# Kernel tuning notes

Hardware: AMD Instinct MI355X
Metric: run time of the kernel (lower is better)

The kernel has to match this reference:

```python
import jax, jax.numpy as jnp
import numpy as np

EPS = 1e-5
K = 9
DILATION = 1

def bn(x, g, b, m, v):
    # x: (B,C,N,1), inference-mode BatchNorm2d with running stats
    sh = (1, -1, 1, 1)
    return (x - m.reshape(sh)) * (g.reshape(sh) / jnp.sqrt(v.reshape(sh) + EPS)) + b.reshape(sh)

def conv1x1(x, w, b):
    # w: (Cout, Cin), x: (B,Cin,N,1)
    return jnp.einsum('oc,bcnj->bonj', w, x) + b.reshape(1, -1, 1, 1)

def knn_idx(feat, k):
    # feat: (B,C,N) -> (B,N,k) indices of k nearest nodes (incl. self)
    xt = jnp.transpose(feat, (0, 2, 1))  # (B,N,C)
    x2 = jnp.sum(xt * xt, axis=-1)       # (B,N)
    dist = x2[:, :, None] - 2.0 * jnp.einsum('bnc,bmc->bnm', xt, xt) + x2[:, None, :]
    _, idx = jax.lax.top_k(-dist, k)
    return idx

def setup_inputs():
    key = jax.random.key(0)
    ks = jax.random.split(key, 24)
    B, C, H, W = 16, 256, 32, 32
    HID = 512
    def g(i, shape, s=1.0):
        return jax.random.normal(ks[i], shape, dtype=jnp.float32) * s
    def pos(i, shape):
        return jax.random.uniform(ks[i], shape, dtype=jnp.float32, minval=0.5, maxval=1.5)
    return {
        'x': g(0, (B, C, H, W)),
        'fc1_w': g(1, (C, C), 0.05), 'fc1_b': g(2, (C,), 0.05),
        'bn1_g': pos(3, (C,)), 'bn1_b': g(4, (C,), 0.1), 'bn1_m': g(5, (C,), 0.1), 'bn1_v': pos(6, (C,)),
        'gc_w': g(7, (HID, 2 * C), 0.05), 'gc_b': g(8, (HID,), 0.05),
        'gbn_g': pos(9, (HID,)), 'gbn_b': g(10, (HID,), 0.1), 'gbn_m': g(11, (HID,), 0.1), 'gbn_v': pos(12, (HID,)),
        'bn2_g': pos(13, (HID,)), 'bn2_b': g(14, (HID,), 0.1), 'bn2_m': g(15, (HID,), 0.1), 'bn2_v': pos(16, (HID,)),
        'fc2_w': g(17, (C, HID), 0.05), 'fc2_b': g(18, (C,), 0.05),
        'bn3_g': pos(19, (C,)), 'bn3_b': g(20, (C,), 0.1), 'bn3_m': g(21, (C,), 0.1), 'bn3_v': pos(22, (C,)),
    }

def reference(x, fc1_w, fc1_b, bn1_g, bn1_b, bn1_m, bn1_v,
              gc_w, gc_b, gbn_g, gbn_b, gbn_m, gbn_v,
              bn2_g, bn2_b, bn2_m, bn2_v,
              fc2_w, fc2_b, bn3_g, bn3_b, bn3_m, bn3_v):
    B, C, H, W = x.shape
    N = H * W
    x = x.reshape(B, C, N, 1)
    shortcut = x
    # fc1: 1x1 conv + BN
    h = bn(conv1x1(x, fc1_w, fc1_b), bn1_g, bn1_b, bn1_m, bn1_v)
    # DyGraphConv2d: dynamic dilated kNN graph over N nodes
    feat = h[..., 0]  # (B,C,N)
    idx = knn_idx(feat, K * DILATION)[:, :, ::DILATION]  # (B,N,K)
    # MRConv2d: max over neighbors of (x_j - x_i)
    x_j = jax.vmap(lambda f, i: f[:, i])(feat, idx)        # (B,C,N,K) gather
    diff_max = jnp.max(x_j - feat[:, :, :, None], axis=-1)  # (B,C,N)
    # interleave [x, max_diff] along channel dim -> (B, 2C, N, 1)
    m = jnp.stack([feat, diff_max], axis=2).reshape(B, 2 * C, N, 1)
    g = conv1x1(m, gc_w, gc_b)
    g = bn(g, gbn_g, gbn_b, gbn_m, gbn_v)  # BasicConv BN, act='None'
    # graph_conv Sequential: BN + GELU (erf, torch default)
    g = jax.nn.gelu(bn(g, bn2_g, bn2_b, bn2_m, bn2_v), approximate=False)
    # fc2 + residual (drop_path=0 -> identity)
    out = bn(conv1x1(g, fc2_w, fc2_b), bn3_g, bn3_b, bn3_m, bn3_v)
    return out + shortcut
```

## Files before the change

### kernel.cpp

```cpp
#include <hip/hip_runtime.h>
#include <hip/hip_bf16.h>
#include <stdint.h>

typedef unsigned long long u64;
typedef __hip_bfloat16 bf16;
typedef short s8v __attribute__((ext_vector_type(8)));
typedef short s4v __attribute__((ext_vector_type(4)));
typedef float f4v __attribute__((ext_vector_type(4)));

#define B_   16
#define C_   256
#define N_   1024
#define HID_ 512

__device__ __forceinline__ unsigned short f2b(float f) {
    unsigned u = __float_as_uint(f);
    unsigned r = (u + 0x7FFFu + ((u >> 16) & 1u)) >> 16;
    return (unsigned short)r;
}
__device__ __forceinline__ float b2f(unsigned short s) {
    return __uint_as_float(((unsigned)s) << 16);
}
__device__ __forceinline__ float ldIn(const void* p, long long i, int bf) {
    return bf ? b2f(((const unsigned short*)p)[i]) : ((const float*)p)[i];
}
__device__ __forceinline__ u64 shfl_xor_u64(u64 v, int m) {
    unsigned lo = (unsigned)v, hi = (unsigned)(v >> 32);
    lo = __shfl_xor(lo, m, 64);
    hi = __shfl_xor(hi, m, 64);
    return ((u64)hi << 32) | lo;
}

__global__ void prep_kernel(const void* xp,
    const void* fc1_b, const void* bn1_g, const void* bn1_b, const void* bn1_m, const void* bn1_v,
    const void* gc_b,  const void* gbn_g, const void* gbn_b, const void* gbn_m, const void* gbn_v,
    const void* bn2_g, const void* bn2_b, const void* bn2_m, const void* bn2_v,
    const void* fc2_b, const void* bn3_g, const void* bn3_b, const void* bn3_m, const void* bn3_v,
    int* flags, float* s1, float* t1, float* Sg, float* Tg, float* s3, float* t3,
    float* x2)
{
    __shared__ int sf;
    if (threadIdx.x == 0) {
        const unsigned short* u = (const unsigned short*)xp;
        int cnt = 0;
        for (int i = 0; i < 64; ++i) {
            int e = (u[2 * i] >> 7) & 0xFF;
            cnt += (e >= 87 && e <= 167);
        }
        int f = (cnt >= 48) ? 1 : 0;
        flags[0] = f;
        sf = f;
    }
    for (int i = threadIdx.x; i < B_ * N_; i += 512) x2[i] = 0.f;
    __syncthreads();
    int bf = sf;
    int i = threadIdx.x;
    if (i < 256) {
        float g = ldIn(bn1_g, i, bf), bb = ldIn(bn1_b, i, bf);
        float m = ldIn(bn1_m, i, bf), v  = ldIn(bn1_v, i, bf);
        float s = g / sqrtf(v + 1e-5f);
        s1[i] = s;
        t1[i] = (ldIn(fc1_b, i, bf) - m) * s + bb;

        float g3 = ldIn(bn3_g, i, bf), b3 = ldIn(bn3_b, i, bf);
        float m3 = ldIn(bn3_m, i, bf), v3 = ldIn(bn3_v, i, bf);
        float ss3 = g3 / sqrtf(v3 + 1e-5f);
        s3[i] = ss3;
        t3[i] = (ldIn(fc2_b, i, bf) - m3) * ss3 + b3;
    }
    if (i < 512) {
        float gg = ldIn(gbn_g, i, bf), gb = ldIn(gbn_b, i, bf);
        float gm = ldIn(gbn_m, i, bf), gv = ldIn(gbn_v, i, bf);
        float sg = gg / sqrtf(gv + 1e-5f);
        float g2 = ldIn(bn2_g, i, bf), b2 = ldIn(bn2_b, i, bf);
        float m2 = ldIn(bn2_m, i, bf), v2 = ldIn(bn2_v, i, bf);
        float s2 = g2 / sqrtf(v2 + 1e-5f);
        Sg[i] = sg * s2;
        Tg[i] = ((ldIn(gc_b, i, bf) - gm) * sg + gb - m2) * s2 + b2;
    }
}

__global__ __launch_bounds__(256)
void cast_weights(const void* w1, const void* wg, const void* w2,
                  short* W1b, short* Wgb, short* W2b, const int* flags)
{
    int inf = flags[0];
    int i = blockIdx.x * 256 + threadIdx.x;
    if (i < 65536) {
        W1b[i] = (short)f2b(ldIn(w1, i, inf));
    } else if (i < 65536 + 262144) {
        int j = i - 65536;
        Wgb[j] = (short)f2b(ldIn(wg, j, inf));
    } else {
        int j = i - 327680;
        W2b[j] = (short)f2b(ldIn(w2, j, inf));
    }
}

__global__ __launch_bounds__(256)
void fc1_valu(const void* __restrict__ Aw, const void* __restrict__ Bx,
              float* __restrict__ Ft, short* __restrict__ Fhi,
              short* __restrict__ Flo, float* __restrict__ x2,
              const float* __restrict__ s1, const float* __restrict__ t1,
              const int* __restrict__ flags)
{
    __shared__ float As[16][68];
    __shared__ float Bs[16][68];
    __shared__ float x2part[16][64];

    int inf = flags[0];
    int b  = blockIdx.z;
    int o0 = blockIdx.y * 64, n0 = blockIdx.x * 64;
    int t  = threadIdx.x;
    int tn = t & 15, to = t >> 4;
    long long bbase = (long long)b * C_ * N_;

    float acc[4][4] = {};

    for (int k0 = 0; k0 < C_; k0 += 16) {
        {
            int l = t * 4;
            int ao = l >> 4, ak = l & 15;
            long long ai = (long long)(o0 + ao) * C_ + k0 + ak;
            As[ak + 0][ao] = ldIn(Aw, ai + 0, inf);
            As[ak + 1][ao] = ldIn(Aw, ai + 1, inf);
            As[ak + 2][ao] = ldIn(Aw, ai + 2, inf);
            As[ak + 3][ao] = ldIn(Aw, ai + 3, inf);
        }
        {
            int l = t * 4;
            int bk = l >> 6, bn = l & 63;
            long long bi = bbase + (long long)(k0 + bk) * N_ + n0 + bn;
            Bs[bk][bn + 0] = ldIn(Bx, bi + 0, inf);
            Bs[bk][bn + 1] = ldIn(Bx, bi + 1, inf);
            Bs[bk][bn + 2] = ldIn(Bx, bi + 2, inf);
            Bs[bk][bn + 3] = ldIn(Bx, bi + 3, inf);
        }
        __syncthreads();
        #pragma unroll
        for (int k = 0; k < 16; ++k) {
            float av[4], bv[4];
            #pragma unroll
            for (int i = 0; i < 4; ++i) av[i] = As[k][to * 4 + i];
            #pragma unroll
            for (int j = 0; j < 4; ++j) bv[j] = Bs[k][tn * 4 + j];
            #pragma unroll
            for (int i = 0; i < 4; ++i)
                #pragma unroll
                for (int j = 0; j < 4; ++j) acc[i][j] += av[i] * bv[j];
        }
        __syncthreads();
    }

    float p2[4] = {};
    #pragma unroll
    for (int i = 0; i < 4; ++i) {
        int o = o0 + to * 4 + i;
        float s = s1[o], tt = t1[o];
        #pragma unroll
        for (int j = 0; j < 4; ++j) {
            int n = n0 + tn * 4 + j;
            float f = acc[i][j] * s + tt;
            long long oi = ((long long)(b << 10) + n) * C_ + o;
            Ft[oi] = f;
            unsigned short h = f2b(f);
            Fhi[oi] = (short)h;
            Flo[oi] = (short)f2b(f - b2f(h));
            p2[j] += f * f;
        }
    }
    #pragma unroll
    for (int j = 0; j < 4; ++j) x2part[to][tn * 4 + j] = p2[j];
    __syncthreads();
    if (t < 64) {
        float s = 0.f;
        #pragma unroll
        for (int r = 0; r < 16; ++r) s += x2part[r][t];
        atomicAdd(&x2[(b << 10) + n0 + t], s);
    }
}

__global__ __launch_bounds__(256)
void gram_topk(const short* __restrict__ Fhi, const short* __restrict__ Flo,
               const float* __restrict__ x2, u64* __restrict__ Part)
{
    __shared__ __align__(16) char ldsbuf[31232];
    short* Ah  = (short*)(ldsbuf);
    short* Al  = (short*)(ldsbuf + 10240);
    short* Bh  = (short*)(ldsbuf + 20480);
    short* Bl  = (short*)(ldsbuf + 25600);
    float* x2s = (float*)(ldsbuf + 30720);
    u64*   mrg  = (u64*)(ldsbuf);
    u64*   mrg2 = (u64*)(ldsbuf + 20480);

    int t = threadIdx.x;
    int q0 = blockIdx.x * 64, mq = blockIdx.y, b = blockIdx.z;
    int wv = t >> 6, ln15 = t & 15, quad = (t >> 4) & 3;

    if (t < 128) x2s[t] = x2[(b << 10) + mq * 128 + t];

    f4v acc[8];
    #pragma unroll
    for (int i = 0; i < 8; ++i) acc[i] = 0.f;

    for (int kc = 0; kc < 8; ++kc) {
        __syncthreads();
        #pragma unroll
        for (int s = 0; s < 6; ++s) {
            int sid = t + s * 256;
            int row = sid >> 2, seg = sid & 3;
            const short* src;
            short* dst;
            int grow;
            if (row < 128)      { dst = &Ah[row * 40 + seg * 8];         grow = mq * 128 + row;       src = Fhi; }
            else if (row < 256) { dst = &Al[(row - 128) * 40 + seg * 8]; grow = mq * 128 + row - 128; src = Flo; }
            else if (row < 320) { dst = &Bh[(row - 256) * 40 + seg * 8]; grow = q0 + row - 256;       src = Fhi; }
            else                { dst = &Bl[(row - 320) * 40 + seg * 8]; grow = q0 + row - 320;       src = Flo; }
            *(s8v*)dst = *(const s8v*)(src + ((long long)((b << 10) + grow)) * C_ + kc * 32 + seg * 8);
        }
        __syncthreads();
        s8v qh = *(s8v*)&Bh[(wv * 16 + ln15) * 40 + quad * 8];
        s8v ql = *(s8v*)&Bl[(wv * 16 + ln15) * 40 + quad * 8];
        #pragma unroll
        for (int i = 0; i < 8; ++i) {
            s8v mh = *(s8v*)&Ah[(i * 16 + ln15) * 40 + quad * 8];
            s8v ml = *(s8v*)&Al[(i * 16 + ln15) * 40 + quad * 8];
            acc[i] = __builtin_amdgcn_mfma_f32_16x16x32_bf16(mh, qh, acc[i], 0, 0, 0);
            acc[i] = __builtin_amdgcn_mfma_f32_16x16x32_bf16(mh, ql, acc[i], 0, 0, 0);
            acc[i] = __builtin_amdgcn_mfma_f32_16x16x32_bf16(ml, qh, acc[i], 0, 0, 0);
        }
    }

    u64 l[9];
    #pragma unroll
    for (int i = 0; i < 9; ++i) l[i] = ~0ULL;
    #pragma unroll
    for (int i = 0; i < 8; ++i) {
        #pragma unroll
        for (int r = 0; r < 4; ++r) {
            int mloc = i * 16 + quad * 4 + r;
            float d = x2s[mloc] - 2.f * acc[i][r];
            unsigned u = __float_as_uint(d);
            u = (u & 0x80000000u) ? ~u : (u | 0x80000000u);
            u64 key = ((u64)u << 32) | (unsigned)(mq * 128 + mloc);
            if (key < l[8]) {
                u64 x = key;
                #pragma unroll
                for (int jj = 0; jj < 9; ++jj) {
                    u64 lo2 = l[jj] < x ? l[jj] : x;
                    u64 hi2 = l[jj] < x ? x : l[jj];
                    l[jj] = lo2; x = hi2;
                }
            }
        }
    }

    __syncthreads();
    {
        int qloc = wv * 16 + ln15;
        #pragma unroll
        for (int k = 0; k < 9; ++k) mrg[(qloc * 4 + quad) * 9 + k] = l[k];
    }
    __syncthreads();
    if (t < 128) {
        int r = t >> 1, pr = t & 1;
        const u64* LA = &mrg[(r * 4 + pr * 2) * 9];
        const u64* LB = LA + 9;
        int ia = 0, ib = 0;
        u64* Po = &mrg2[(r * 2 + pr) * 9];
        #pragma unroll
        for (int k = 0; k < 9; ++k) {
            u64 va = LA[ia], vb = LB[ib];
            bool ta = va < vb;
            Po[k] = ta ? va : vb;
            ia += ta; ib += !ta;
        }
    }
    __syncthreads();
    if (t < 64) {
        const u64* LA = &mrg2[(t * 2) * 9];
        const u64* LB = LA + 9;
        int ia = 0, ib = 0;
        u64* P = Part + (((long long)((b << 10) + q0 + t)) * 8 + mq) * 9;
        #pragma unroll
        for (int k = 0; k < 9; ++k) {
            u64 va = LA[ia], vb = LB[ib];
            bool ta = va < vb;
            P[k] = ta ? va : vb;
            ia += ta; ib += !ta;
        }
    }
}

__global__ __launch_bounds__(256)
void build_Mt(const float* __restrict__ Ft, const u64* __restrict__ Part,
              short* __restrict__ Mt)
{
    int t = threadIdx.x;
    int wv = t >> 6, lane = t & 63;
    int n = blockIdx.x * 4 + wv;
    int b = blockIdx.y;
    long long nb = (long long)(b << 10) + n;

    const u64* L = Part + nb * 72 + (long long)(lane & 7) * 9;
    u64 l[9];
    #pragma unroll
    for (int k = 0; k < 9; ++k) l[k] = L[k];
    #pragma unroll
    for (int s = 1; s <= 4; s <<= 1) {
        u64 p[9];
        #pragma unroll
        for (int k = 0; k < 9; ++k) p[k] = shfl_xor_u64(l[k], s);
        #pragma unroll
        for (int k = 0; k < 9; ++k) {
            u64 x = p[k];
            if (x < l[8]) {
                #pragma unroll
                for (int jj = 0; jj < 9; ++jj) {
                    u64 lo2 = l[jj] < x ? l[jj] : x;
                    u64 hi2 = l[jj] < x ? x : l[jj];
                    l[jj] = lo2; x = hi2;
                }
            }
        }
    }

    int c0 = lane * 4;
    f4v f = *(const f4v*)(Ft + nb * C_ + c0);
    f4v mx = {-3.4e38f, -3.4e38f, -3.4e38f, -3.4e38f};
    #pragma unroll
    for (int k = 0; k < 9; ++k) {
        int id = (int)(l[k] & 0xFFFFFFFFu);
        f4v g = *(const f4v*)(Ft + ((long long)(b << 10) + id) * C_ + c0);
        mx[0] = fmaxf(mx[0], g[0]); mx[1] = fmaxf(mx[1], g[1]);
        mx[2] = fmaxf(mx[2], g[2]); mx[3] = fmaxf(mx[3], g[3]);
    }
    s8v m8;
    #pragma unroll
    for (int r = 0; r < 4; ++r) {
        m8[2 * r]     = (short)f2b(f[r]);
        m8[2 * r + 1] = (short)f2b(mx[r] - f[r]);
    }
    *(s8v*)(Mt + nb * (2 * C_) + 2 * c0) = m8;
}

template<int EPI>
__global__ __launch_bounds__(256)
void mfma_gemm(const short* __restrict__ A, const short* __restrict__ Bm,
               void* __restrict__ Out, const float* __restrict__ scale,
               const float* __restrict__ bias, const void* __restrict__ resid,
               const int* __restrict__ flags, int K, int Odim)
{
    __shared__ short As[128][40];
    __shared__ short Bs[128][40];

    int t = threadIdx.x, b = blockIdx.z;
    int n0 = blockIdx.x * 128, o0 = blockIdx.y * 128;
    int wv = t >> 6, ln = t & 15, quad = (t >> 4) & 3;
    int wo = (wv & 1) * 64, wn = (wv >> 1) * 64;

    f4v acc[4][4];
    #pragma unroll
    for (int i = 0; i < 4; ++i)
        #pragma unroll
        for (int j = 0; j < 4; ++j) acc[i][j] = 0.f;

    const short* Ab = A + (long long)o0 * K;
    const short* Bb = Bm + ((long long)(b << 10) + n0) * K;

    for (int k0 = 0; k0 < K; k0 += 32) {
        __syncthreads();
        #pragma unroll
        for (int s = 0; s < 2; ++s) {
            int sid = t + s * 256;
            int row = sid >> 2, seg = sid & 3;
            *(s8v*)&As[row][seg * 8] = *(const s8v*)(Ab + (long long)row * K + k0 + seg * 8);
            *(s8v*)&Bs[row][seg * 8] = *(const s8v*)(Bb + (long long)row * K + k0 + seg * 8);
        }
        __syncthreads();
        s8v a[4], bf[4];
        #pragma unroll
        for (int i = 0; i < 4; ++i) a[i]  = *(s8v*)&As[wo + i * 16 + ln][quad * 8];
        #pragma unroll
        for (int j = 0; j < 4; ++j) bf[j] = *(s8v*)&Bs[wn + j * 16 + ln][quad * 8];
        #pragma unroll
        for (int i = 0; i < 4; ++i)
            #pragma unroll
            for (int j = 0; j < 4; ++j)
                acc[i][j] = __builtin_amdgcn_mfma_f32_16x16x32_bf16(a[i], bf[j], acc[i][j], 0, 0, 0);
    }

    int inf = flags[0];
    #pragma unroll
    for (int i = 0; i < 4; ++i) {
        int ob = o0 + wo + i * 16 + quad * 4;
        #pragma unroll
        for (int j = 0; j < 4; ++j) {
            int n = n0 + wn + j * 16 + ln;
            f4v v = acc[i][j];
            if (EPI == 0) {
                s4v g;
                #pragma unroll
                for (int r = 0; r < 4; ++r) {
                    float val = v[r] * scale[ob + r] + bias[ob + r];
                    val = 0.5f * val * (1.0f + erff(val * 0.70710678118654752f));
                    g[r] = (short)f2b(val);
                }
                *(s4v*)((short*)Out + ((long long)(b << 10) + n) * Odim + ob) = g;
            } else {
                #pragma unroll
                for (int r = 0; r < 4; ++r) {
                    int o = ob + r;
                    long long oi = ((long long)b * Odim + o) * N_ + n;
                    ((float*)Out)[oi] = v[r] * scale[o] + bias[o] + ldIn(resid, oi, inf);
                }
            }
        }
    }
}

extern "C" void kernel_launch(void* const* d_in, const int* in_sizes, int n_in,
                              void* d_out, int out_size, void* d_ws, size_t ws_size,
                              hipStream_t stream)
{
    const void* p[23];
    if (n_in >= 23 && in_sizes[0] != 4194304 && in_sizes[22] == 4194304) {
        const int amap[23] = {
            22, 13, 12, 1, 0, 2, 3,
            21, 20, 17, 16, 18, 19,
            5, 4, 6, 7,
            15, 14, 9, 8, 10, 11 };
        for (int i = 0; i < 23; ++i) p[i] = d_in[amap[i]];
    } else {
        for (int i = 0; i < 23; ++i) p[i] = d_in[i];
    }

    const void* x     = p[0];
    const void* fc1_w = p[1];
    const void* fc1_b = p[2];
    const void* bn1_g = p[3];
    const void* bn1_b = p[4];
    const void* bn1_m = p[5];
    const void* bn1_v = p[6];
    const void* gc_w  = p[7];
    const void* gc_b  = p[8];
    const void* gbn_g = p[9];
    const void* gbn_b = p[10];
    const void* gbn_m = p[11];
    const void* gbn_v = p[12];
    const void* bn2_g = p[13];
    const void* bn2_b = p[14];
    const void* bn2_m = p[15];
    const void* bn2_v = p[16];
    const void* fc2_w = p[17];
    const void* fc2_b = p[18];
    const void* bn3_g = p[19];
    const void* bn3_b = p[20];
    const void* bn3_m = p[21];
    const void* bn3_v = p[22];

    char* ws = (char*)d_ws;
    size_t off = 0;
    int*   flags = (int*)ws;
    float* s1 = (float*)(ws + 256);
    float* t1 = s1 + 256;
    float* s3 = t1 + 256;
    float* t3 = s3 + 256;
    float* Sg = t3 + 256;
    float* Tg = Sg + 512;
    off = 16384;
    short* W1b   = (short*)(ws + off); off += (size_t)C_ * C_ * 2;
    short* Wgb   = (short*)(ws + off); off += (size_t)HID_ * 2 * C_ * 2;
    short* W2b   = (short*)(ws + off); off += (size_t)C_ * HID_ * 2;
    float* Ft    = (float*)(ws + off); off += (size_t)B_ * N_ * C_ * 4;
    short* Fhi   = (short*)(ws + off); off += (size_t)B_ * N_ * C_ * 2;
    short* Flo   = (short*)(ws + off); off += (size_t)B_ * N_ * C_ * 2;
    float* x2    = (float*)(ws + off); off += (size_t)B_ * N_ * 4;
    u64*   Part  = (u64*)  (ws + off); off += (size_t)B_ * N_ * 8 * 9 * 8;
    short* Mt    = (short*)(ws + off); off += (size_t)B_ * N_ * 2 * C_ * 2;
    short* Gt    = (short*)(ws + off); off += (size_t)B_ * N_ * HID_ * 2;

    prep_kernel<<<1, 512, 0, stream>>>(x,
        fc1_b, bn1_g, bn1_b, bn1_m, bn1_v,
        gc_b, gbn_g, gbn_b, gbn_m, gbn_v,
        bn2_g, bn2_b, bn2_m, bn2_v,
        fc2_b, bn3_g, bn3_b, bn3_m, bn3_v,
        flags, s1, t1, Sg, Tg, s3, t3, x2);

    cast_weights<<<1792, 256, 0, stream>>>(fc1_w, gc_w, fc2_w,
                                           W1b, Wgb, W2b, flags);

    fc1_valu<<<dim3(16, 4, B_), 256, 0, stream>>>(
        fc1_w, x, Ft, Fhi, Flo, x2, s1, t1, flags);

    gram_topk<<<dim3(16, 8, 16), 256, 0, stream>>>(Fhi, Flo, x2, Part);

    build_Mt<<<dim3(256, 16), 256, 0, stream>>>(Ft, Part, Mt);

    mfma_gemm<0><<<dim3(8, 4, 16), 256, 0, stream>>>(
        Wgb, Mt, Gt, Sg, Tg, nullptr, flags, 2 * C_, HID_);

    mfma_gemm<1><<<dim3(8, 2, 16), 256, 0, stream>>>(
        W2b, Gt, d_out, s3, t3, x, flags, HID_, C_);
}
```

Measured before the change: 336.6 us.

## Merge prep and weight cast, split F conversion, shrink MFMA GEMM tiles

Folds the BN-parameter prep and the weight casting into one multi-block kernel and drops the unused fc1 bf16 weight cast. The hi/lo bf16 split and squared-norm computation move out of the fc1 epilogue into a separate vectorized kernel that uses a wave reduction, which removes the atomics and the x2 zeroing. The MFMA GEMMs go from 128x128 tiles to 64x64 tiles, one 16-column slice per wave, launched over four times as many blocks. This buys more parallelism and fewer registers, at the cost of much less operand reuse per block and an extra read of Ft.

```diff
diff --git a/kernel.cpp b/kernel.cpp
--- a/kernel.cpp
+++ b/kernel.cpp
@@ -30,83 +30,78 @@
     hi = __shfl_xor(hi, m, 64);
     return ((u64)hi << 32) | lo;
 }
-
-__global__ void prep_kernel(const void* xp,
+__device__ __forceinline__ int probe_bf16(const void* xp) {
+    const unsigned short* u = (const unsigned short*)xp;
+    int cnt = 0;
+    for (int i = 0; i < 64; ++i) {
+        int e = (u[2 * i] >> 7) & 0xFF;
+        cnt += (e >= 87 && e <= 167);
+    }
+    return (cnt >= 48) ? 1 : 0;
+}
+
+__global__ __launch_bounds__(256)
+void prep_cast(const void* xp,
+    const void* wg, const void* w2,
     const void* fc1_b, const void* bn1_g, const void* bn1_b, const void* bn1_m, const void* bn1_v,
     const void* gc_b,  const void* gbn_g, const void* gbn_b, const void* gbn_m, const void* gbn_v,
     const void* bn2_g, const void* bn2_b, const void* bn2_m, const void* bn2_v,
     const void* fc2_b, const void* bn3_g, const void* bn3_b, const void* bn3_m, const void* bn3_v,
     int* flags, float* s1, float* t1, float* Sg, float* Tg, float* s3, float* t3,
-    float* x2)
+    short* Wgb, short* W2b)
 {
     __shared__ int sf;
-    if (threadIdx.x == 0) {
-        const unsigned short* u = (const unsigned short*)xp;
-        int cnt = 0;
-        for (int i = 0; i < 64; ++i) {
-            int e = (u[2 * i] >> 7) & 0xFF;
-            cnt += (e >= 87 && e <= 167);
-        }
-        int f = (cnt >= 48) ? 1 : 0;
-        flags[0] = f;
-        sf = f;
-    }
-    for (int i = threadIdx.x; i < B_ * N_; i += 512) x2[i] = 0.f;
+    int t = threadIdx.x, blk = blockIdx.x;
+    if (t == 0) sf = probe_bf16(xp);
     __syncthreads();
     int bf = sf;
-    int i = threadIdx.x;
-    if (i < 256) {
-        float g = ldIn(bn1_g, i, bf), bb = ldIn(bn1_b, i, bf);
-        float m = ldIn(bn1_m, i, bf), v  = ldIn(bn1_v, i, bf);
-        float s = g / sqrtf(v + 1e-5f);
-        s1[i] = s;
-        t1[i] = (ldIn(fc1_b, i, bf) - m) * s + bb;
-
-        float g3 = ldIn(bn3_g, i, bf), b3 = ldIn(bn3_b, i, bf);
-        float m3 = ldIn(bn3_m, i, bf), v3 = ldIn(bn3_v, i, bf);
-        float ss3 = g3 / sqrtf(v3 + 1e-5f);
-        s3[i] = ss3;
-        t3[i] = (ldIn(fc2_b, i, bf) - m3) * ss3 + b3;
-    }
-    if (i < 512) {
-        float gg = ldIn(gbn_g, i, bf), gb = ldIn(gbn_b, i, bf);
-        float gm = ldIn(gbn_m, i, bf), gv = ldIn(gbn_v, i, bf);
-        float sg = gg / sqrtf(gv + 1e-5f);
-        float g2 = ldIn(bn2_g, i, bf), b2 = ldIn(bn2_b, i, bf);
-        float m2 = ldIn(bn2_m, i, bf), v2 = ldIn(bn2_v, i, bf);
-        float s2 = g2 / sqrtf(v2 + 1e-5f);
-        Sg[i] = sg * s2;
-        Tg[i] = ((ldIn(gc_b, i, bf) - gm) * sg + gb - m2) * s2 + b2;
-    }
-}
-
-__global__ __launch_bounds__(256)
-void cast_weights(const void* w1, const void* wg, const void* w2,
-                  short* W1b, short* Wgb, short* W2b, const int* flags)
-{
-    int inf = flags[0];
-    int i = blockIdx.x * 256 + threadIdx.x;
-    if (i < 65536) {
-        W1b[i] = (short)f2b(ldIn(w1, i, inf));
-    } else if (i < 65536 + 262144) {
-        int j = i - 65536;
-        Wgb[j] = (short)f2b(ldIn(wg, j, inf));
-    } else {
-        int j = i - 327680;
-        W2b[j] = (short)f2b(ldIn(w2, j, inf));
+
+    if (blk == 0) {
+        if (t == 0) flags[0] = bf;
+        for (int i = t; i < 512; i += 256) {
+            if (i < 256) {
+                float g = ldIn(bn1_g, i, bf), bb = ldIn(bn1_b, i, bf);
+                float m = ldIn(bn1_m, i, bf), v  = ldIn(bn1_v, i, bf);
+                float s = g / sqrtf(v + 1e-5f);
+                s1[i] = s;
+                t1[i] = (ldIn(fc1_b, i, bf) - m) * s + bb;
+
+                float g3 = ldIn(bn3_g, i, bf), b3 = ldIn(bn3_b, i, bf);
+                float m3 = ldIn(bn3_m, i, bf), v3 = ldIn(bn3_v, i, bf);
+                float ss3 = g3 / sqrtf(v3 + 1e-5f);
+                s3[i] = ss3;
+                t3[i] = (ldIn(fc2_b, i, bf) - m3) * ss3 + b3;
+            }
+            float gg = ldIn(gbn_g, i, bf), gb = ldIn(gbn_b, i, bf);
+            float gm = ldIn(gbn_m, i, bf), gv = ldIn(gbn_v, i, bf);
+            float sg = gg / sqrtf(gv + 1e-5f);
+            float g2 = ldIn(bn2_g, i, bf), b2 = ldIn(bn2_b, i, bf);
+            float m2 = ldIn(bn2_m, i, bf), v2 = ldIn(bn2_v, i, bf);
+            float s2 = g2 / sqrtf(v2 + 1e-5f);
+            Sg[i] = sg * s2;
+            Tg[i] = ((ldIn(gc_b, i, bf) - gm) * sg + gb - m2) * s2 + b2;
+        }
+    }
+
+    #pragma unroll
+    for (int e = 0; e < 2; ++e) {
+        int i = (blk * 256 + t) * 2 + e;
+        if (i < 262144) {
+            Wgb[i] = (short)f2b(ldIn(wg, i, bf));
+        } else if (i < 393216) {
+            int j = i - 262144;
+            W2b[j] = (short)f2b(ldIn(w2, j, bf));
+        }
     }
 }
 
 __global__ __launch_bounds__(256)
 void fc1_valu(const void* __restrict__ Aw, const void* __restrict__ Bx,
-              float* __restrict__ Ft, short* __restrict__ Fhi,
-              short* __restrict__ Flo, float* __restrict__ x2,
-              const float* __restrict__ s1, const float* __restrict__ t1,
-              const int* __restrict__ flags)
+              float* __restrict__ Ft, const float* __restrict__ s1,
+              const float* __restrict__ t1, const int* __restrict__ flags)
 {
     __shared__ float As[16][68];
     __shared__ float Bs[16][68];
-    __shared__ float x2part[16][64];
 
     int inf = flags[0];
     int b  = blockIdx.z;
@@ -152,7 +147,6 @@
         __syncthreads();
     }
 
-    float p2[4] = {};
     #pragma unroll
     for (int i = 0; i < 4; ++i) {
         int o = o0 + to * 4 + i;
@@ -160,24 +154,36 @@
         #pragma unroll
         for (int j = 0; j < 4; ++j) {
             int n = n0 + tn * 4 + j;
-            float f = acc[i][j] * s + tt;
-            long long oi = ((long long)(b << 10) + n) * C_ + o;
-            Ft[oi] = f;
-            unsigned short h = f2b(f);
-            Fhi[oi] = (short)h;
-            Flo[oi] = (short)f2b(f - b2f(h));
-            p2[j] += f * f;
-        }
-    }
-    #pragma unroll
-    for (int j = 0; j < 4; ++j) x2part[to][tn * 4 + j] = p2[j];
-    __syncthreads();
-    if (t < 64) {
-        float s = 0.f;
-        #pragma unroll
-        for (int r = 0; r < 16; ++r) s += x2part[r][t];
-        atomicAdd(&x2[(b << 10) + n0 + t], s);
-    }
+            Ft[((long long)(b << 10) + n) * C_ + o] = acc[i][j] * s + tt;
+        }
+    }
+}
+
+__global__ __launch_bounds__(256)
+void prep_F(const float* __restrict__ Ft, short* __restrict__ Fhi,
+            short* __restrict__ Flo, float* __restrict__ x2)
+{
+    int t = threadIdx.x;
+    int wv = t >> 6, lane = t & 63;
+    int n = blockIdx.x * 4 + wv;
+    int b = blockIdx.y;
+    long long base = ((long long)(b << 10) + n) * C_ + lane * 4;
+    f4v f = *(const f4v*)(Ft + base);
+
+    s4v hi, lo;
+    #pragma unroll
+    for (int r = 0; r < 4; ++r) {
+        unsigned short h = f2b(f[r]);
+        hi[r] = (short)h;
+        lo[r] = (short)f2b(f[r] - b2f(h));
+    }
+    *(s4v*)(Fhi + base) = hi;
+    *(s4v*)(Flo + base) = lo;
+
+    float ss = f[0]*f[0] + f[1]*f[1] + f[2]*f[2] + f[3]*f[3];
+    #pragma unroll
+    for (int s = 32; s >= 1; s >>= 1) ss += __shfl_xor(ss, s, 64);
+    if (lane == 0) x2[(b << 10) + n] = ss;
 }
 
 __global__ __launch_bounds__(256)
@@ -351,69 +357,60 @@
                const float* __restrict__ bias, const void* __restrict__ resid,
                const int* __restrict__ flags, int K, int Odim)
 {
-    __shared__ short As[128][40];
-    __shared__ short Bs[128][40];
+    __shared__ __align__(16) short As[64 * 40];
+    __shared__ __align__(16) short Bs[64 * 40];
 
     int t = threadIdx.x, b = blockIdx.z;
-    int n0 = blockIdx.x * 128, o0 = blockIdx.y * 128;
-    int wv = t >> 6, ln = t & 15, quad = (t >> 4) & 3;
-    int wo = (wv & 1) * 64, wn = (wv >> 1) * 64;
-
-    f4v acc[4][4];
-    #pragma unroll
-    for (int i = 0; i < 4; ++i)
-        #pragma unroll
-        for (int j = 0; j < 4; ++j) acc[i][j] = 0.f;
-
-    const short* Ab = A + (long long)o0 * K;
-    const short* Bb = Bm + ((long long)(b << 10) + n0) * K;
-
-    for (int k0 = 0; k0 < K; k0 += 32) {
+    int n0 = blockIdx.x * 64, o0 = blockIdx.y * 64;
+    int wv = t >> 6, ln15 = t & 15, quad = (t >> 4) & 3;
+
+    f4v acc[4];
+    #pragma unroll
+    for (int i = 0; i < 4; ++i) acc[i] = 0.f;
+
+    int nkc = K >> 5;
+    for (int kc = 0; kc < nkc; ++kc) {
         __syncthreads();
         #pragma unroll
         for (int s = 0; s < 2; ++s) {
             int sid = t + s * 256;
-            int row = sid >> 2, seg = sid & 3;
-            *(s8v*)&As[row][seg * 8] = *(const s8v*)(Ab + (long long)row * K + k0 + seg * 8);
-            *(s8v*)&Bs[row][seg * 8] = *(const s8v*)(Bb + (long long)row * K + k0 + seg * 8);
+            int row = (sid >> 2) & 63, seg = sid & 3;
+            if (s == 0)
+                *(s8v*)&As[row * 40 + seg * 8] =
+                    *(const s8v*)(A + (long long)(o0 + row) * K + kc * 32 + seg * 8);
+            else
+                *(s8v*)&Bs[row * 40 + seg * 8] =
+                    *(const s8v*)(Bm + ((long long)((b << 10) + n0 + row)) * K + kc * 32 + seg * 8);
         }
         __syncthreads();
-        s8v a[4], bf[4];
-        #pragma unroll
-        for (int i = 0; i < 4; ++i) a[i]  = *(s8v*)&As[wo + i * 16 + ln][quad * 8];
-        #pragma unroll
-        for (int j = 0; j < 4; ++j) bf[j] = *(s8v*)&Bs[wn + j * 16 + ln][quad * 8];
-        #pragma unroll
-        for (int i = 0; i < 4; ++i)
+        s8v bf = *(s8v*)&Bs[(wv * 16 + ln15) * 40 + quad * 8];
+        #pragma unroll
+        for (int i = 0; i < 4; ++i) {
+            s8v a = *(s8v*)&As[(i * 16 + ln15) * 40 + quad * 8];
+            acc[i] = __builtin_amdgcn_mfma_f32_16x16x32_bf16(a, bf, acc[i], 0, 0, 0);
+        }
+    }
+
+    int inf = flags[0];
+    int n = n0 + wv * 16 + ln15;
+    #pragma unroll
+    for (int i = 0; i < 4; ++i) {
+        int ob = o0 + i * 16 + quad * 4;
+        if (EPI == 0) {
+            s4v g;
             #pragma unroll
-            for (int j = 0; j < 4; ++j)
-                acc[i][j] = __builtin_amdgcn_mfma_f32_16x16x32_bf16(a[i], bf[j], acc[i][j], 0, 0, 0);
-    }
-
-    int inf = flags[0];
-    #pragma unroll
-    for (int i = 0; i < 4; ++i) {
-        int ob = o0 + wo + i * 16 + quad * 4;
-        #pragma unroll
-        for (int j = 0; j < 4; ++j) {
-            int n = n0 + wn + j * 16 + ln;
-            f4v v = acc[i][j];
-            if (EPI == 0) {
-                s4v g;
-                #pragma unroll
-                for (int r = 0; r < 4; ++r) {
-                    float val = v[r] * scale[ob + r] + bias[ob + r];
-                    val = 0.5f * val * (1.0f + erff(val * 0.70710678118654752f));
-                    g[r] = (short)f2b(val);
-                }
-                *(s4v*)((short*)Out + ((long long)(b << 10) + n) * Odim + ob) = g;
-            } else {
-                #pragma unroll
-                for (int r = 0; r < 4; ++r) {
-                    int o = ob + r;
-                    long long oi = ((long long)b * Odim + o) * N_ + n;
-                    ((float*)Out)[oi] = v[r] * scale[o] + bias[o] + ldIn(resid, oi, inf);
-                }
+            for (int r = 0; r < 4; ++r) {
+                float val = acc[i][r] * scale[ob + r] + bias[ob + r];
+                val = 0.5f * val * (1.0f + erff(val * 0.70710678118654752f));
+                g[r] = (short)f2b(val);
+            }
+            *(s4v*)((short*)Out + ((long long)((b << 10) + n)) * Odim + ob) = g;
+        } else {
+            #pragma unroll
+            for (int r = 0; r < 4; ++r) {
+                int o = ob + r;
+                long long oi = ((long long)b * Odim + o) * N_ + n;
+                ((float*)Out)[oi] = acc[i][r] * scale[o] + bias[o] + ldIn(resid, oi, inf);
             }
         }
     }
@@ -469,7 +466,6 @@
     float* Sg = t3 + 256;
     float* Tg = Sg + 512;
     off = 16384;
-    short* W1b   = (short*)(ws + off); off += (size_t)C_ * C_ * 2;
     short* Wgb   = (short*)(ws + off); off += (size_t)HID_ * 2 * C_ * 2;
     short* W2b   = (short*)(ws + off); off += (size_t)C_ * HID_ * 2;
     float* Ft    = (float*)(ws + off); off += (size_t)B_ * N_ * C_ * 4;
@@ -480,26 +476,26 @@
     short* Mt    = (short*)(ws + off); off += (size_t)B_ * N_ * 2 * C_ * 2;
     short* Gt    = (short*)(ws + off); off += (size_t)B_ * N_ * HID_ * 2;
 
-    prep_kernel<<<1, 512, 0, stream>>>(x,
+    prep_cast<<<768, 256, 0, stream>>>(x,
+        gc_w, fc2_w,
         fc1_b, bn1_g, bn1_b, bn1_m, bn1_v,
         gc_b, gbn_g, gbn_b, gbn_m, gbn_v,
         bn2_g, bn2_b, bn2_m, bn2_v,
         fc2_b, bn3_g, bn3_b, bn3_m, bn3_v,
-        flags, s1, t1, Sg, Tg, s3, t3, x2);
-
-    cast_weights<<<1792, 256, 0, stream>>>(fc1_w, gc_w, fc2_w,
-                                           W1b, Wgb, W2b, flags);
-
-    fc1_valu<<<dim3(16, 4, B_), 256, 0, stream>>>(
-        fc1_w, x, Ft, Fhi, Flo, x2, s1, t1, flags);
+        flags, s1, t1, Sg, Tg, s3, t3,
+        Wgb, W2b);
+
+    fc1_valu<<<dim3(16, 4, B_), 256, 0, stream>>>(fc1_w, x, Ft, s1, t1, flags);
+
+    prep_F<<<dim3(N_ / 4, B_), 256, 0, stream>>>(Ft, Fhi, Flo, x2);
 
     gram_topk<<<dim3(16, 8, 16), 256, 0, stream>>>(Fhi, Flo, x2, Part);
 
     build_Mt<<<dim3(256, 16), 256, 0, stream>>>(Ft, Part, Mt);
 
-    mfma_gemm<0><<<dim3(8, 4, 16), 256, 0, stream>>>(
+    mfma_gemm<0><<<dim3(16, 8, 16), 256, 0, stream>>>(
         Wgb, Mt, Gt, Sg, Tg, nullptr, flags, 2 * C_, HID_);
 
-    mfma_gemm<1><<<dim3(8, 2, 16), 256, 0, stream>>>(
+    mfma_gemm<1><<<dim3(16, 4, 16), 256, 0, stream>>>(
         W2b, Gt, d_out, s3, t3, x, flags, HID_, C_);
 }
```

Measured after the change: 320.4 us. 4.8% less time.
